# Performance work log

Measured on AMD Instinct MI355X. Metric: run time of the kernel, lower is better.

Reference implementation:

```python
import jax, jax.numpy as jnp
import numpy as np

N = 1024       # sample size
ZC = 64        # z_c dim
ZD = 64        # z_d dim
H = ZC         # FF hidden dim = zc_dim per InfoNCE.__init__


def setup_inputs() -> dict:
    key = jax.random.key(0)
    ks = jax.random.split(key, 6)
    s1 = 1.0 / np.sqrt(ZC + ZD)
    s2 = 1.0 / np.sqrt(H)
    return {
        "z_c": jax.random.normal(ks[0], (N, ZC), jnp.float32),
        "z_d": jax.random.normal(ks[1], (N, ZD), jnp.float32),
        # FF params: Linear(ZC+ZD,H) -> relu -> Linear(H,H) -> relu -> Linear(H,1)
        "W1": jax.random.normal(ks[2], (ZC + ZD, H), jnp.float32) * s1,
        "b1": jnp.zeros((H,), jnp.float32),
        "W2": jax.random.normal(ks[3], (H, H), jnp.float32) * s2,
        "b2": jnp.zeros((H,), jnp.float32),
        "Wo": jax.random.normal(ks[4], (H, 1), jnp.float32) * s2,
        "bo": jnp.zeros((1,), jnp.float32),
    }


def reference(z_c, z_d, W1, b1, W2, b2, Wo, bo):
    n = z_d.shape[0]
    zc_dim = z_c.shape[-1]

    # T0: critic on matched pairs, input concat([z_c, z_d]) -> [N, 1]
    x0 = jnp.concatenate([z_c, z_d], axis=-1)
    h0 = jax.nn.relu(x0 @ W1 + b1)
    h0 = jax.nn.relu(h0 @ W2 + b2)
    T0 = h0 @ Wo + bo  # [N, 1]

    # T1: critic on all NxN pairs. Instead of materializing the tiled
    # concat [N, N, ZC+ZD], decompose the first linear layer:
    # concat([zc_tile, zd_tile]) @ W1 == zc_tile @ W1c + zd_tile @ W1d.
    # zc_tile[i, j] = z_c[j], zd_tile[i, j] = z_d[i]  (exact same math).
    W1c, W1d = W1[:zc_dim], W1[zc_dim:]
    h1 = jax.nn.relu((z_c @ W1c)[None, :, :] + (z_d @ W1d)[:, None, :] + b1)  # [N, N, H]
    h2 = jax.nn.relu(h1 @ W2 + b2)                                            # [N, N, H]
    T1 = (h2 @ Wo + bo)[..., 0]                                               # [N, N]

    lower_bound = T0.mean() - (jax.nn.logsumexp(T1, axis=1).mean() - jnp.log(jnp.float32(n)))
    return lower_bound
```

## Files before the change

### kernel.cpp

```cpp
#include <hip/hip_runtime.h>
#include <hip/hip_fp16.h>
#include <math.h>

#define NN 1024

typedef _Float16 half8 __attribute__((ext_vector_type(8)));
typedef float f32x4 __attribute__((ext_vector_type(4)));

union H8U { uint4 u; half8 h; };

__device__ __forceinline__ unsigned short h_bits(float x) {
    _Float16 h = (_Float16)x;
    unsigned short b;
    __builtin_memcpy(&b, &h, 2);
    return b;
}

__global__ void prep_kernel(const float* __restrict__ z_c, const float* __restrict__ z_d,
                            const float* __restrict__ W1, const float* __restrict__ b1,
                            const float* __restrict__ W2,
                            unsigned short* __restrict__ Aph,
                            unsigned short* __restrict__ Bph,
                            uint4* __restrict__ W2h,
                            float* __restrict__ Srow) {
    if (blockIdx.x < 512) {
        int t = blockIdx.x * 256 + threadIdx.x;
        int sel = t >> 16;
        int idx = t & 0xffff;
        int n = idx >> 6, h = idx & 63;
        const float* z = (sel ? z_d : z_c) + n * 64;
        const float* w = W1 + (sel ? 4096 : 0) + h;
        float a0 = sel ? 0.f : b1[h], a1 = 0.f;
        #pragma unroll
        for (int k = 0; k < 64; k += 2) {
            a0 = fmaf(z[k],     w[k * 64],       a0);
            a1 = fmaf(z[k + 1], w[(k + 1) * 64], a1);
        }
        unsigned short val = h_bits(a0 + a1);
        int s = h >> 5, q = (h >> 3) & 3, e = h & 7;
        if (sel) {
            Bph[n * 64 + q * 16 + s * 8 + e] = val;
        } else {
            Aph[(n >> 4) * 1024 + (q * 16 + (n & 15)) * 16 + s * 8 + e] = val;
        }
    } else {
        int tt = (blockIdx.x - 512) * 256 + threadIdx.x;
        Srow[tt] = 0.f; Srow[tt + 512] = 0.f;
        int f = tt >> 6, lane = tt & 63;
        int s = f >> 2, t4 = f & 3, q = lane >> 4, l15 = lane & 15;
        int n = t4 * 16 + l15;
        unsigned w4[4];
        #pragma unroll
        for (int p = 0; p < 4; ++p) {
            int k = s * 32 + q * 8 + 2 * p;
            unsigned lo = h_bits(W2[k * 64 + n]);
            unsigned hi = h_bits(W2[(k + 1) * 64 + n]);
            w4[p] = lo | (hi << 16);
        }
        W2h[f * 64 + lane] = make_uint4(w4[0], w4[1], w4[2], w4[3]);
    }
}

__global__ void __launch_bounds__(256, 4)
main_kernel(const unsigned short* __restrict__ Aph, const unsigned short* __restrict__ Bph,
            const uint4* __restrict__ W2h,
            const float* __restrict__ b2, const float* __restrict__ Wo,
            float* __restrict__ Srow, float* __restrict__ T0row) {
    const int i       = blockIdx.x >> 2;
    const int quarter = blockIdx.x & 3;
    const int lane = threadIdx.x & 63;
    const int wave = threadIdx.x >> 6;
    const int l15  = lane & 15;
    const int q    = lane >> 4;

    half8 W[2][4];
    #pragma unroll
    for (int f = 0; f < 8; ++f) {
        H8U u; u.u = W2h[f * 64 + lane];
        W[f >> 2][f & 3] = u.h;
    }

    H8U cb0, cb1;
    {
        const uint4* bp = (const uint4*)(Bph + i * 64 + q * 16);
        cb0.u = bp[0];
        cb1.u = bp[1];
    }

    f32x4 b2v[4];
    float wov[4][4];
    #pragma unroll
    for (int t = 0; t < 4; ++t) {
        float4 bt = *(const float4*)(b2 + t * 16 + q * 4);
        float4 wt = *(const float4*)(Wo + t * 16 + q * 4);
        b2v[t] = (f32x4){bt.x, bt.y, bt.z, bt.w};
        wov[t][0] = wt.x; wov[t][1] = wt.y; wov[t][2] = wt.z; wov[t][3] = wt.w;
    }

    const int tbase = quarter * 16 + wave * 4;
    const unsigned short* ap = Aph + tbase * 1024 + lane * 16;

    H8U x0, x1;
    x0.u = ((const uint4*)ap)[0];
    x1.u = ((const uint4*)ap)[1];

    const half8 zero = {0, 0, 0, 0, 0, 0, 0, 0};
    float psum[4];
    float sacc = 0.f;

    #pragma unroll
    for (int tile = 0; tile < 4; ++tile) {
        half8 a0 = __builtin_elementwise_max(x0.h + cb0.h, zero);
        half8 a1 = __builtin_elementwise_max(x1.h + cb1.h, zero);
        if (tile < 3) {
            const uint4* nx = (const uint4*)(ap + (tile + 1) * 1024);
            x0.u = nx[0];
            x1.u = nx[1];
        }

        f32x4 acc[4];
        #pragma unroll
        for (int t = 0; t < 4; ++t) acc[t] = b2v[t];
        #pragma unroll
        for (int t = 0; t < 4; ++t) {
            acc[t] = __builtin_amdgcn_mfma_f32_16x16x32_f16(W[0][t], a0, acc[t], 0, 0, 0);
            acc[t] = __builtin_amdgcn_mfma_f32_16x16x32_f16(W[1][t], a1, acc[t], 0, 0, 0);
        }

        float p0 = 0.f, p1 = 0.f, p2 = 0.f, p3 = 0.f;
        #pragma unroll
        for (int t = 0; t < 4; ++t) {
            p0 = fmaf(fmaxf(acc[t][0], 0.f), wov[t][0], p0);
            p1 = fmaf(fmaxf(acc[t][1], 0.f), wov[t][1], p1);
            p2 = fmaf(fmaxf(acc[t][2], 0.f), wov[t][2], p2);
            p3 = fmaf(fmaxf(acc[t][3], 0.f), wov[t][3], p3);
        }
        psum[tile] = (p0 + p1) + (p2 + p3);
    }

    #pragma unroll
    for (int tile = 0; tile < 4; ++tile) {
        float ps = psum[tile];
        ps += __shfl_xor(ps, 16);
        ps += __shfl_xor(ps, 32);
        const int j = (tbase + tile) * 16 + l15;
        if (j == i && q == 0) T0row[i] = ps;
        sacc += __expf(ps);
    }
    sacc += __shfl_xor(sacc, 1);
    sacc += __shfl_xor(sacc, 2);
    sacc += __shfl_xor(sacc, 4);
    sacc += __shfl_xor(sacc, 8);
    if (lane == 0) atomicAdd(&Srow[i], sacc);
}

__global__ void __launch_bounds__(1024)
combine_finish(const float* __restrict__ Srow, const float* __restrict__ T0row,
               float* __restrict__ out) {
    int i = threadIdx.x;
    float l  = logf(Srow[i]);
    float t0 = T0row[i];
    #pragma unroll
    for (int off = 1; off < 64; off <<= 1) {
        l  += __shfl_xor(l, off);
        t0 += __shfl_xor(t0, off);
    }
    __shared__ float sl[16], st[16];
    int w = threadIdx.x >> 6;
    if ((threadIdx.x & 63) == 0) { sl[w] = l; st[w] = t0; }
    __syncthreads();
    if (threadIdx.x == 0) {
        float L = 0.f, T = 0.f;
        #pragma unroll
        for (int k = 0; k < 16; ++k) { L += sl[k]; T += st[k]; }
        out[0] = (T - L) * (1.0f / 1024.0f) + 6.9314718055994531f;
    }
}

extern "C" void kernel_launch(void* const* d_in, const int* in_sizes, int n_in,
                              void* d_out, int out_size, void* d_ws, size_t ws_size,
                              hipStream_t stream) {
    const float* z_c = (const float*)d_in[0];
    const float* z_d = (const float*)d_in[1];
    const float* W1  = (const float*)d_in[2];
    const float* b1  = (const float*)d_in[3];
    const float* W2  = (const float*)d_in[4];
    const float* b2  = (const float*)d_in[5];
    const float* Wo  = (const float*)d_in[6];
    float* out   = (float*)d_out;

    unsigned short* Aph = (unsigned short*)d_ws;
    unsigned short* Bph = Aph + NN * 64;
    uint4* W2h  = (uint4*)(Bph + NN * 64);
    float* Srow = (float*)(W2h + 512);
    float* T0row = Srow + NN;

    prep_kernel<<<514, 256, 0, stream>>>(z_c, z_d, W1, b1, W2, Aph, Bph, W2h, Srow);
    main_kernel<<<4096, 256, 0, stream>>>(Aph, Bph, W2h, b2, Wo, Srow, T0row);
    combine_finish<<<1, 1024, 0, stream>>>(Srow, T0row, out);
}
```

Before: 99.67 us.

## Fuse final logsumexp reduction into main kernel via completion counters

Drops the separate single-block combine kernel. Each wave now bumps a per-row counter after adding its partial sum. The last of the 16 waves for a row adds log(S_row) into a global accumulator, and the last row to finish writes the final output. T0 is accumulated atomically instead of stored per row. This removes one kernel launch and its dependency gap, at the cost of extra atomics and non-deterministic float summation order.

Result: slower. 362.1 us (+263.3%).

```diff
diff --git a/kernel.cpp b/kernel.cpp
--- a/kernel.cpp
+++ b/kernel.cpp
@@ -22,7 +22,10 @@
                             unsigned short* __restrict__ Aph,
                             unsigned short* __restrict__ Bph,
                             uint4* __restrict__ W2h,
-                            float* __restrict__ Srow) {
+                            float* __restrict__ Srow,
+                            unsigned* __restrict__ cnt,
+                            float* __restrict__ accum,
+                            unsigned* __restrict__ rows_done) {
     if (blockIdx.x < 512) {
         int t = blockIdx.x * 256 + threadIdx.x;
         int sel = t >> 16;
@@ -46,6 +49,10 @@
     } else {
         int tt = (blockIdx.x - 512) * 256 + threadIdx.x;
         Srow[tt] = 0.f; Srow[tt + 512] = 0.f;
+        cnt[tt] = 0u;  cnt[tt + 512] = 0u;
+        if (blockIdx.x == 512 && threadIdx.x == 0) {
+            accum[0] = 0.f; accum[1] = 0.f; rows_done[0] = 0u;
+        }
         int f = tt >> 6, lane = tt & 63;
         int s = f >> 2, t4 = f & 3, q = lane >> 4, l15 = lane & 15;
         int n = t4 * 16 + l15;
@@ -65,7 +72,9 @@
 main_kernel(const unsigned short* __restrict__ Aph, const unsigned short* __restrict__ Bph,
             const uint4* __restrict__ W2h,
             const float* __restrict__ b2, const float* __restrict__ Wo,
-            float* __restrict__ Srow, float* __restrict__ T0row) {
+            float* __restrict__ Srow, unsigned* __restrict__ cnt,
+            float* __restrict__ accum, unsigned* __restrict__ rows_done,
+            float* __restrict__ out) {
     const int i       = blockIdx.x >> 2;
     const int quarter = blockIdx.x & 3;
     const int lane = threadIdx.x & 63;
@@ -144,36 +153,34 @@
         ps += __shfl_xor(ps, 16);
         ps += __shfl_xor(ps, 32);
         const int j = (tbase + tile) * 16 + l15;
-        if (j == i && q == 0) T0row[i] = ps;
+        if (j == i && q == 0)
+            __hip_atomic_fetch_add(&accum[0], ps, __ATOMIC_RELAXED,
+                                   __HIP_MEMORY_SCOPE_AGENT);
         sacc += __expf(ps);
     }
     sacc += __shfl_xor(sacc, 1);
     sacc += __shfl_xor(sacc, 2);
     sacc += __shfl_xor(sacc, 4);
     sacc += __shfl_xor(sacc, 8);
-    if (lane == 0) atomicAdd(&Srow[i], sacc);
-}
-
-__global__ void __launch_bounds__(1024)
-combine_finish(const float* __restrict__ Srow, const float* __restrict__ T0row,
-               float* __restrict__ out) {
-    int i = threadIdx.x;
-    float l  = logf(Srow[i]);
-    float t0 = T0row[i];
-    #pragma unroll
-    for (int off = 1; off < 64; off <<= 1) {
-        l  += __shfl_xor(l, off);
-        t0 += __shfl_xor(t0, off);
-    }
-    __shared__ float sl[16], st[16];
-    int w = threadIdx.x >> 6;
-    if ((threadIdx.x & 63) == 0) { sl[w] = l; st[w] = t0; }
-    __syncthreads();
-    if (threadIdx.x == 0) {
-        float L = 0.f, T = 0.f;
-        #pragma unroll
-        for (int k = 0; k < 16; ++k) { L += sl[k]; T += st[k]; }
-        out[0] = (T - L) * (1.0f / 1024.0f) + 6.9314718055994531f;
+
+    if (lane == 0) {
+        __hip_atomic_fetch_add(&Srow[i], sacc, __ATOMIC_RELAXED, __HIP_MEMORY_SCOPE_AGENT);
+        unsigned prev = __hip_atomic_fetch_add(&cnt[i], 1u, __ATOMIC_ACQ_REL,
+                                               __HIP_MEMORY_SCOPE_AGENT);
+        if (prev == 15u) {
+            float s = __hip_atomic_load(&Srow[i], __ATOMIC_RELAXED, __HIP_MEMORY_SCOPE_AGENT);
+            __hip_atomic_fetch_add(&accum[1], logf(s), __ATOMIC_RELAXED,
+                                   __HIP_MEMORY_SCOPE_AGENT);
+            unsigned rd = __hip_atomic_fetch_add(rows_done, 1u, __ATOMIC_ACQ_REL,
+                                                 __HIP_MEMORY_SCOPE_AGENT);
+            if (rd == 1023u) {
+                float t0 = __hip_atomic_load(&accum[0], __ATOMIC_RELAXED,
+                                             __HIP_MEMORY_SCOPE_AGENT);
+                float L  = __hip_atomic_load(&accum[1], __ATOMIC_RELAXED,
+                                             __HIP_MEMORY_SCOPE_AGENT);
+                out[0] = (t0 - L) * (1.0f / 1024.0f) + 6.9314718055994531f;
+            }
+        }
     }
 }
 
@@ -191,11 +198,14 @@
 
     unsigned short* Aph = (unsigned short*)d_ws;
     unsigned short* Bph = Aph + NN * 64;
-    uint4* W2h  = (uint4*)(Bph + NN * 64);
-    float* Srow = (float*)(W2h + 512);
-    float* T0row = Srow + NN;
-
-    prep_kernel<<<514, 256, 0, stream>>>(z_c, z_d, W1, b1, W2, Aph, Bph, W2h, Srow);
-    main_kernel<<<4096, 256, 0, stream>>>(Aph, Bph, W2h, b2, Wo, Srow, T0row);
-    combine_finish<<<1, 1024, 0, stream>>>(Srow, T0row, out);
-}
+    uint4* W2h   = (uint4*)(Bph + NN * 64);
+    float* Srow  = (float*)(W2h + 512);
+    unsigned* cnt = (unsigned*)(Srow + NN);
+    float* accum = (float*)(cnt + NN);
+    unsigned* rows_done = (unsigned*)(accum + 8);
+
+    prep_kernel<<<514, 256, 0, stream>>>(z_c, z_d, W1, b1, W2, Aph, Bph, W2h,
+                                         Srow, cnt, accum, rows_done);
+    main_kernel<<<4096, 256, 0, stream>>>(Aph, Bph, W2h, b2, Wo,
+                                          Srow, cnt, accum, rows_done, out);
+}
```
